# Kernel tuning notes

Measured on AMD Instinct MI355X. Metric: run time of the kernel, lower is better.

The kernel has to match this reference:

```python
import jax, jax.numpy as jnp
import numpy as np

KERNEL = 2
STRIDE = 2
V_MAX = 6.0
# Derived fuzzy constants (match torch module)
_C = V_MAX / 4.0          # 1.5  center of mu1
_D = V_MAX / 2.0          # 3.0  -> width1 = d - c = 1.5
_A = 1.5                  # width of mu2
_M = V_MAX / 2.0          # 3.0  center of mu2
_R = V_MAX / 2.0          # 3.0  center of mu3
_Q = _R + V_MAX / 4.0     # 4.5  -> width3 = q - r = 1.5


def setup_inputs() -> dict:
    key = jax.random.key(0)
    # inputs scaled to [0, v_max) like post-activation feature maps
    x = jax.random.uniform(key, (32, 64, 128, 128), dtype=jnp.float32) * V_MAX
    return {"x": x}


def _tri(v, center, width):
    return jnp.clip(1.0 - jnp.abs(v - center) / width, 0.0, None)


def reference(x):
    B, C, H, W = x.shape
    Ho, Wo = (H - KERNEL) // STRIDE + 1, (W - KERNEL) // STRIDE + 1
    # stride == kernel: non-overlapping patches via reshape
    # (B,C,Ho,k,Wo,k) -> (B,C,Ho,Wo,k*k)
    p = x.reshape(B, C, Ho, KERNEL, Wo, KERNEL)
    p = p.transpose(0, 1, 2, 4, 3, 5).reshape(B, C, Ho, Wo, KERNEL * KERNEL)

    mu = jnp.stack([
        _tri(p, _C, _D - _C),
        _tri(p, _M, _A),
        _tri(p, _R, _Q - _R),
    ], axis=0)                      # (3, B, C, Ho, Wo, K)
    s_vals = mu.sum(axis=-1)        # (3, B, C, Ho, Wo)
    sel = jnp.argmax(s_vals, axis=0)                     # (B, C, Ho, Wo)
    mu_sel = jnp.take_along_axis(mu, sel[None, ..., None], axis=0)[0]  # (B,C,Ho,Wo,K)

    num = jnp.sum(mu_sel * p * p, axis=-1)
    den = jnp.sum(mu_sel * p, axis=-1)
    safe_den = jnp.where(den == 0.0, 1.0, den)
    return jnp.where(den == 0.0, 0.0, num / safe_den)
```

## Files before the change

kernel.cpp:

```cpp
#include <hip/hip_runtime.h>

#define H_IN 128
#define W_IN 128
#define H_OUT 64
#define W_OUT 64

__device__ __forceinline__ float tri_mu(float v, float c) {
    return fmaxf(1.0f - fabsf(v - c) / 1.5f, 0.0f);
}

__device__ __forceinline__ float fuzzy4(float p0, float p1, float p2, float p3) {
    float a0 = tri_mu(p0, 1.5f), a1 = tri_mu(p1, 1.5f), a2 = tri_mu(p2, 1.5f), a3 = tri_mu(p3, 1.5f);
    float b0 = tri_mu(p0, 3.0f), b1 = tri_mu(p1, 3.0f), b2 = tri_mu(p2, 3.0f), b3 = tri_mu(p3, 3.0f);

    float s1 = ((a0 + a1) + a2) + a3;
    float s2 = ((b0 + b1) + b2) + b3;

    float u0, u1, u2, u3;
    if (s1 >= s2) {
        u0 = a0; u1 = a1; u2 = a2; u3 = a3;
    } else {
        u0 = b0; u1 = b1; u2 = b2; u3 = b3;
    }

    float t0 = u0 * p0, t1 = u1 * p1, t2 = u2 * p2, t3 = u3 * p3;
    float num = ((t0 * p0 + t1 * p1) + t2 * p2) + t3 * p3;
    float den = ((t0 + t1) + t2) + t3;
    return (den == 0.0f) ? 0.0f : num / den;
}

__global__ __launch_bounds__(256) void fuzzy_pool_kernel(
        const float* __restrict__ x, float* __restrict__ out, int n_pairs) {
    int gid = blockIdx.x * blockDim.x + threadIdx.x;
    if (gid >= n_pairs) return;

    int row = gid >> 5;
    int pw  = gid & 31;
    int bc  = row >> 6;
    int ho  = row & 63;

    const float* r0 = x + (size_t)bc * (H_IN * W_IN) + (size_t)(2 * ho) * W_IN + pw * 4;
    const float* r1 = r0 + W_IN;

    float4 top = *(const float4*)r0;
    float4 bot = *(const float4*)r1;

    float2 o;
    o.x = fuzzy4(top.x, top.y, bot.x, bot.y);
    o.y = fuzzy4(top.z, top.w, bot.z, bot.w);

    *(float2*)(out + (size_t)row * W_OUT + pw * 2) = o;
}

extern "C" void kernel_launch(void* const* d_in, const int* in_sizes, int n_in,
                              void* d_out, int out_size, void* d_ws, size_t ws_size,
                              hipStream_t stream) {
    const float* x = (const float*)d_in[0];
    float* out = (float*)d_out;

    int n_pairs = out_size / 2;
    int block = 256;
    int grid = (n_pairs + block - 1) / block;
    fuzzy_pool_kernel<<<grid, block, 0, stream>>>(x, out, n_pairs);
}
```

Measured before the change: 194.3 us.

## Process four outputs per thread with nontemporal vector loads and cheaper math

Each thread now handles eight input columns and writes four outputs, using nontemporal 16-byte loads and stores. Division by 1.5 becomes an FMA with the reciprocal, the final divide uses a hardware reciprocal, and the branch-based selection becomes selects. The aim is to cut per-thread overhead and cache pollution in this memory-bound streaming kernel. The approximate reciprocal and the changed rounding may cause small numerical differences.

```diff
diff --git a/kernel.cpp b/kernel.cpp
--- a/kernel.cpp
+++ b/kernel.cpp
@@ -5,8 +5,10 @@
 #define H_OUT 64
 #define W_OUT 64
 
+typedef float vf4 __attribute__((ext_vector_type(4)));
+
 __device__ __forceinline__ float tri_mu(float v, float c) {
-    return fmaxf(1.0f - fabsf(v - c) / 1.5f, 0.0f);
+    return fmaxf(fmaf(fabsf(v - c), -0.66666666666666667f, 1.0f), 0.0f);
 }
 
 __device__ __forceinline__ float fuzzy4(float p0, float p1, float p2, float p3) {
@@ -16,40 +18,44 @@
     float s1 = ((a0 + a1) + a2) + a3;
     float s2 = ((b0 + b1) + b2) + b3;
 
-    float u0, u1, u2, u3;
-    if (s1 >= s2) {
-        u0 = a0; u1 = a1; u2 = a2; u3 = a3;
-    } else {
-        u0 = b0; u1 = b1; u2 = b2; u3 = b3;
-    }
+    bool sel1 = (s1 >= s2);
+    float u0 = sel1 ? a0 : b0;
+    float u1 = sel1 ? a1 : b1;
+    float u2 = sel1 ? a2 : b2;
+    float u3 = sel1 ? a3 : b3;
 
     float t0 = u0 * p0, t1 = u1 * p1, t2 = u2 * p2, t3 = u3 * p3;
     float num = ((t0 * p0 + t1 * p1) + t2 * p2) + t3 * p3;
     float den = ((t0 + t1) + t2) + t3;
-    return (den == 0.0f) ? 0.0f : num / den;
+    float r = __builtin_amdgcn_rcpf(den);
+    return (den == 0.0f) ? 0.0f : num * r;
 }
 
 __global__ __launch_bounds__(256) void fuzzy_pool_kernel(
-        const float* __restrict__ x, float* __restrict__ out, int n_pairs) {
+        const float* __restrict__ x, float* __restrict__ out, int n_quads) {
     int gid = blockIdx.x * blockDim.x + threadIdx.x;
-    if (gid >= n_pairs) return;
+    if (gid >= n_quads) return;
 
-    int row = gid >> 5;
-    int pw  = gid & 31;
+    int row = gid >> 4;
+    int qw  = gid & 15;
     int bc  = row >> 6;
     int ho  = row & 63;
 
-    const float* r0 = x + (size_t)bc * (H_IN * W_IN) + (size_t)(2 * ho) * W_IN + pw * 4;
+    const float* r0 = x + (size_t)bc * (H_IN * W_IN) + (size_t)(2 * ho) * W_IN + qw * 8;
     const float* r1 = r0 + W_IN;
 
-    float4 top = *(const float4*)r0;
-    float4 bot = *(const float4*)r1;
+    vf4 ta = __builtin_nontemporal_load((const vf4*)r0);
+    vf4 tb = __builtin_nontemporal_load((const vf4*)r0 + 1);
+    vf4 ba = __builtin_nontemporal_load((const vf4*)r1);
+    vf4 bb = __builtin_nontemporal_load((const vf4*)r1 + 1);
 
-    float2 o;
-    o.x = fuzzy4(top.x, top.y, bot.x, bot.y);
-    o.y = fuzzy4(top.z, top.w, bot.z, bot.w);
+    vf4 o;
+    o.x = fuzzy4(ta.x, ta.y, ba.x, ba.y);
+    o.y = fuzzy4(ta.z, ta.w, ba.z, ba.w);
+    o.z = fuzzy4(tb.x, tb.y, bb.x, bb.y);
+    o.w = fuzzy4(tb.z, tb.w, bb.z, bb.w);
 
-    *(float2*)(out + (size_t)row * W_OUT + pw * 2) = o;
+    __builtin_nontemporal_store(o, (vf4*)(out + (size_t)row * W_OUT + qw * 4));
 }
 
 extern "C" void kernel_launch(void* const* d_in, const int* in_sizes, int n_in,
@@ -58,8 +64,8 @@
     const float* x = (const float*)d_in[0];
     float* out = (float*)d_out;
 
-    int n_pairs = out_size / 2;
+    int n_quads = out_size / 4;
     int block = 256;
-    int grid = (n_pairs + block - 1) / block;
-    fuzzy_pool_kernel<<<grid, block, 0, stream>>>(x, out, n_pairs);
+    int grid = (n_quads + block - 1) / block;
+    fuzzy_pool_kernel<<<grid, block, 0, stream>>>(x, out, n_quads);
 }
```

New measurement: 186.1 us. 1.04x faster.
